# Optimization experiments

Measured on AMD Instinct MI355X. Metric: run time of the kernel, lower is better.

## Reference

```python
import jax, jax.numpy as jnp
import numpy as np

B, S, D = 4, 2048, 1024
H = 16
HD = D // H  # 64


def setup_inputs() -> dict:
    key = jax.random.key(0)
    kx, kq, kp = jax.random.split(key, 3)
    x = jax.random.normal(kx, (B, S, D), dtype=jnp.float32)
    # torch Linear weights are [out, in]; match init scale ~ U(-1/sqrt(in), 1/sqrt(in))
    lim = 1.0 / np.sqrt(D)
    w_qkv = jax.random.uniform(kq, (3 * D, D), dtype=jnp.float32, minval=-lim, maxval=lim)
    w_proj = jax.random.uniform(kp, (D, D), dtype=jnp.float32, minval=-lim, maxval=lim)
    return {"x": x, "w_qkv": w_qkv, "w_proj": w_proj}


def reference(x, w_qkv, w_proj):
    b, s, d = x.shape
    qkv = jnp.einsum('bsd,ed->bse', x, w_qkv)  # [B,S,3D]
    q, k, v = jnp.split(qkv, 3, axis=-1)
    # [B,H,S,HD]
    q = q.reshape(b, s, H, HD).transpose(0, 2, 1, 3)
    k = k.reshape(b, s, H, HD).transpose(0, 2, 1, 3)
    v = v.reshape(b, s, H, HD).transpose(0, 2, 1, 3)
    scale = 1.0 / np.sqrt(HD)
    attn = jnp.einsum('bhqd,bhkd->bhqk', q, k) * scale  # [B,H,S,S]
    causal = jnp.tril(jnp.ones((s, s), dtype=bool))
    attn = jnp.where(causal[None, None], attn, -jnp.inf)
    attn = jax.nn.softmax(attn, axis=-1)
    out = jnp.einsum('bhqk,bhkd->bhqd', attn, v)
    out = out.transpose(0, 2, 1, 3).reshape(b, s, d)
    return jnp.einsum('bsd,ed->bse', out, w_proj)
```

## Files before the change

kernel.cpp:

```cpp
#include <hip/hip_runtime.h>

typedef unsigned short u16;
typedef unsigned int u32;

#define B_ 4
#define S_ 2048
#define D_ 1024
#define H_ 16
#define HD_ 64
#define M_ (B_ * S_)
#define QK_ (2 * D_)
#define NP_ 32

typedef __bf16 bf16x8 __attribute__((ext_vector_type(8)));
typedef float f32x4 __attribute__((ext_vector_type(4)));

#define MASKVAL (-1.0e30f)
#define RESCALE_THR 8.0f

static __device__ __forceinline__ u16 f2bf_hw(float f) {
    union { __bf16 b; u16 u; } v;
    v.b = (__bf16)f;
    return v.u;
}

static __device__ __forceinline__ void gload16(const u16* g, u16* l) {
    __builtin_amdgcn_global_load_lds(
        (const __attribute__((address_space(1))) void*)g,
        (__attribute__((address_space(3))) void*)l, 16, 0, 0);
}

__global__ __launch_bounds__(256) void cvt_bf16(const float* __restrict__ src,
                                                u16* __restrict__ dst) {
    size_t i = ((size_t)blockIdx.x * 256 + threadIdx.x) * 8;
    float4 a = *(const float4*)(src + i);
    float4 b = *(const float4*)(src + i + 4);
    union { u16 h[8]; int4 v; } pk;
    pk.h[0] = f2bf_hw(a.x); pk.h[1] = f2bf_hw(a.y);
    pk.h[2] = f2bf_hw(a.z); pk.h[3] = f2bf_hw(a.w);
    pk.h[4] = f2bf_hw(b.x); pk.h[5] = f2bf_hw(b.y);
    pk.h[6] = f2bf_hw(b.z); pk.h[7] = f2bf_hw(b.w);
    *(int4*)(dst + i) = pk.v;
}

template <int EPI, int BM, int TPB>
__global__ __launch_bounds__(TPB, (TPB == 512) ? 4 : 2)
void gemm8p(const u16* __restrict__ A, const u16* __restrict__ Bw,
            void* __restrict__ Cout, void* __restrict__ C2, int Ndim) {
    __shared__ u16 As[3][BM * 32];
    __shared__ u16 Bs[3][128 * 32];
    constexpr int LA = (BM * 4) / TPB;
    constexpr int LB = 512 / TPB;
    constexpr int L = LA + LB;
    const int t = threadIdx.x;
    const int wave = t >> 6, lane = t & 63;
    const int ml = lane & 15, quad = lane >> 4;
    const int wr = wave >> 1, wc = wave & 1;
    const int bx = blockIdx.x, by = blockIdx.y;
    const int rowA0 = by * BM, rowB0 = bx * 128;

    f32x4 acc[4][4];
    const f32x4 zero = {0.f, 0.f, 0.f, 0.f};
#pragma unroll
    for (int i = 0; i < 4; ++i)
#pragma unroll
        for (int j = 0; j < 4; ++j) acc[i][j] = zero;

    auto STAGE = [&](int slot, int pnl) {
        const int colbase = pnl * 32;
#pragma unroll
        for (int l = 0; l < LA; ++l) {
            const int base = l * TPB + wave * 64;
            const int idx = base + lane;
            const int row = idx >> 2;
            const int sch = ((idx & 3) ^ ((idx >> 3) & 3)) * 8;
            gload16(&A[(size_t)(rowA0 + row) * 1024 + colbase + sch],
                    &As[slot][base * 8]);
        }
#pragma unroll
        for (int l = 0; l < LB; ++l) {
            const int base = l * TPB + wave * 64;
            const int idx = base + lane;
            const int row = idx >> 2;
            const int sch = ((idx & 3) ^ ((idx >> 3) & 3)) * 8;
            gload16(&Bw[(size_t)(rowB0 + row) * 1024 + colbase + sch],
                    &Bs[slot][base * 8]);
        }
    };

    STAGE(0, 0);
    STAGE(1, 1);
    if constexpr (L == 3) { asm volatile("s_waitcnt vmcnt(3)" ::: "memory"); }
    else                  { asm volatile("s_waitcnt vmcnt(4)" ::: "memory"); }
    __builtin_amdgcn_s_barrier();

    for (int p = 0; p < NP_; ++p) {
        const int slot = p % 3;
        bf16x8 a[4], b[4];
#pragma unroll
        for (int i = 0; i < 4; ++i) {
            const int row = wr * 64 + i * 16 + ml;
            a[i] = *(const bf16x8*)(&As[slot][row * 32 + ((quad ^ ((row >> 1) & 3)) << 3)]);
        }
#pragma unroll
        for (int j = 0; j < 4; ++j) {
            const int row = wc * 64 + j * 16 + ml;
            b[j] = *(const bf16x8*)(&Bs[slot][row * 32 + ((quad ^ ((row >> 1) & 3)) << 3)]);
        }
        if (p + 2 < NP_) STAGE((p + 2) % 3, p + 2);
        __builtin_amdgcn_s_barrier();
        asm volatile("s_waitcnt lgkmcnt(0)" ::: "memory");
        __builtin_amdgcn_sched_barrier(0);
        __builtin_amdgcn_s_setprio(1);
#pragma unroll
        for (int i = 0; i < 4; ++i)
#pragma unroll
            for (int j = 0; j < 4; ++j)
                acc[i][j] = __builtin_amdgcn_mfma_f32_16x16x32_bf16(a[i], b[j], acc[i][j], 0, 0, 0);
        __builtin_amdgcn_s_setprio(0);
        if (p + 2 < NP_) {
            if constexpr (L == 3) { asm volatile("s_waitcnt vmcnt(3)" ::: "memory"); }
            else                  { asm volatile("s_waitcnt vmcnt(4)" ::: "memory"); }
        } else {
            asm volatile("s_waitcnt vmcnt(0)" ::: "memory");
        }
        __builtin_amdgcn_s_barrier();
    }

    if constexpr (EPI == 2) {
        float* C = (float*)Cout;
#pragma unroll
        for (int i = 0; i < 4; ++i)
#pragma unroll
            for (int j = 0; j < 4; ++j)
#pragma unroll
                for (int r = 0; r < 4; ++r) {
                    int row = rowA0 + wr * 64 + i * 16 + quad * 4 + r;
                    int col = rowB0 + wc * 64 + j * 16 + ml;
                    C[(size_t)row * Ndim + col] = acc[i][j][r];
                }
    } else {
        if (bx < 16) {
            u16* C = (u16*)Cout;
#pragma unroll
            for (int i = 0; i < 4; ++i)
#pragma unroll
                for (int j = 0; j < 4; ++j)
#pragma unroll
                    for (int r = 0; r < 4; ++r) {
                        int row = rowA0 + wr * 64 + i * 16 + quad * 4 + r;
                        int col = rowB0 + wc * 64 + j * 16 + ml;
                        C[(size_t)row * Ndim + col] = f2bf_hw(acc[i][j][r]);
                    }
        } else {
            u16* Vt = (u16*)C2;
#pragma unroll
            for (int i = 0; i < 4; ++i)
#pragma unroll
                for (int j = 0; j < 4; ++j) {
                    int row0 = rowA0 + wr * 64 + i * 16 + quad * 4;
                    int col = rowB0 + wc * 64 + j * 16 + ml - 2048;
                    int b = row0 >> 11;
                    int s0 = row0 & (S_ - 1);
                    union { u16 h[4]; ushort4 v; } pk;
#pragma unroll
                    for (int r = 0; r < 4; ++r) pk.h[r] = f2bf_hw(acc[i][j][r]);
                    *(ushort4*)(&Vt[((size_t)(b * D_ + col)) * S_ + s0]) = pk.v;
                }
        }
    }
}

__global__ __launch_bounds__(256, 3) void attn3(const u16* __restrict__ qk,
                                                const u16* __restrict__ Vt,
                                                u16* __restrict__ AO) {
    __shared__ u16 Klds[2][64 * 64];
    __shared__ u16 Vlds[2][64 * 64];
    __shared__ u16 Pw[4][32 * 72];
    const int t = threadIdx.x;
    const int wave = t >> 6, lane = t & 63;
    const int ml = lane & 15, quad = lane >> 4;
    const int mhx = (ml & 8) >> 1;

    const int jj = blockIdx.x >> 6;
    const int bh = blockIdx.x & 63;
    const int t4 = jj >> 2, r4 = jj & 3;
    const int j = (t4 < 2) ? (15 - 4 * t4 - r4) : (12 - 4 * t4 + r4);
    const int b = bh >> 4, h = bh & 15;
    const size_t rowbase = (size_t)b * S_;

    const int srow8 = lane >> 3;
    const int schunk = ((lane & 7) ^ srow8) * 8;

    const int qj0 = j * 128 + wave * 32;
    const int ktw = 2 * j + (wave >> 1);
    const int ktmax = 2 * j + 1;

    u16* pwb = &Pw[wave][0];

    bf16x8 qf[2][2];
#pragma unroll
    for (int mi = 0; mi < 2; ++mi)
#pragma unroll
        for (int kc = 0; kc < 2; ++kc) {
            bf16x8 q = *(const bf16x8*)(&qk[(rowbase + qj0 + mi * 16 + ml) * QK_ +
                                            h * HD_ + kc * 32 + quad * 8]);
#pragma unroll
            for (int e = 0; e < 8; ++e) {
                float f = (float)q[e] * 0.125f;
                q[e] = (__bf16)f;
            }
            qf[mi][kc] = q;
        }

    f32x4 o[2][4];
    float m[2], ls[2];
    const f32x4 zero = {0.f, 0.f, 0.f, 0.f};
#pragma unroll
    for (int mi = 0; mi < 2; ++mi) {
#pragma unroll
        for (int nd = 0; nd < 4; ++nd) o[mi][nd] = zero;
        m[mi] = MASKVAL; ls[mi] = 0.f;
    }

    bf16x8 vf[4][2];

    auto STAGE = [&](int buf, int kt) {
        const int kb = kt * 64;
#pragma unroll
        for (int p = 0; p < 2; ++p) {
            const int rbase = wave * 16 + p * 8;
            gload16(&qk[(rowbase + kb + rbase + srow8) * QK_ + D_ + h * HD_ + schunk],
                    &Klds[buf][rbase * 64]);
            gload16(&Vt[(size_t)(bh * HD_ + rbase + srow8) * S_ + kb + schunk],
                    &Vlds[buf][rbase * 64]);
        }
    };

    auto PV = [&]() {
        bf16x8 pf[2][2];
#pragma unroll
        for (int mi = 0; mi < 2; ++mi)
#pragma unroll
            for (int kc = 0; kc < 2; ++kc)
                pf[mi][kc] = *(const bf16x8*)(&pwb[(mi * 16 + ml) * 72 +
                                                   (((kc * 4 + quad) ^ mhx) << 3)]);
        __builtin_amdgcn_s_setprio(1);
#pragma unroll
        for (int mi = 0; mi < 2; ++mi)
#pragma unroll
            for (int nd = 0; nd < 4; ++nd)
#pragma unroll
                for (int kc = 0; kc < 2; ++kc)
                    o[mi][nd] = __builtin_amdgcn_mfma_f32_16x16x32_bf16(pf[mi][kc], vf[nd][kc],
                                                                        o[mi][nd], 0, 0, 0);
        __builtin_amdgcn_s_setprio(0);
    };

    STAGE(0, 0);

    for (int kt = 0; kt <= ktmax; ++kt) {
        const int cur = kt & 1;
        if (kt < ktmax) STAGE(cur ^ 1, kt + 1);

        if (kt >= 1 && kt - 1 <= ktw) PV();

        if (kt < ktmax) {
            asm volatile("s_waitcnt vmcnt(4)" ::: "memory");
        } else {
            asm volatile("s_waitcnt vmcnt(0)" ::: "memory");
        }
        __builtin_amdgcn_s_barrier();

        if (kt <= ktw) {
            const int kb = kt * 64;
            f32x4 sc[2][4];
            __builtin_amdgcn_s_setprio(1);
#pragma unroll
            for (int ni = 0; ni < 4; ++ni) {
                const int row = ni * 16 + ml;
                bf16x8 kfa = *(const bf16x8*)(&Klds[cur][row * 64 + ((quad ^ (ml & 7)) << 3)]);
                bf16x8 kfb = *(const bf16x8*)(&Klds[cur][row * 64 + (((4 + quad) ^ (ml & 7)) << 3)]);
#pragma unroll
                for (int mi = 0; mi < 2; ++mi) {
                    f32x4 s = __builtin_amdgcn_mfma_f32_16x16x32_bf16(kfa, qf[mi][0], zero, 0, 0, 0);
                    sc[mi][ni] = __builtin_amdgcn_mfma_f32_16x16x32_bf16(kfb, qf[mi][1], s, 0, 0, 0);
                }
            }
            __builtin_amdgcn_s_setprio(0);

            if (kb + 63 > qj0) {
#pragma unroll
                for (int mi = 0; mi < 2; ++mi) {
                    const int q = qj0 + mi * 16 + ml;
#pragma unroll
                    for (int ni = 0; ni < 4; ++ni)
#pragma unroll
                        for (int r = 0; r < 4; ++r) {
                            int k = kb + ni * 16 + quad * 4 + r;
                            if (k > q) sc[mi][ni][r] = MASKVAL;
                        }
                }
            }

#pragma unroll
            for (int mi = 0; mi < 2; ++mi) {
                float tm = sc[mi][0][0];
#pragma unroll
                for (int ni = 0; ni < 4; ++ni)
#pragma unroll
                    for (int r = 0; r < 4; ++r) tm = fmaxf(tm, sc[mi][ni][r]);
                tm = fmaxf(tm, __shfl_xor(tm, 16, 64));
                tm = fmaxf(tm, __shfl_xor(tm, 32, 64));
                if (__any(tm > m[mi] + RESCALE_THR)) {
                    float mn = fmaxf(m[mi], tm);
                    float al = __expf(m[mi] - mn);
                    m[mi] = mn;
                    ls[mi] *= al;
                    float alr[4];
#pragma unroll
                    for (int r = 0; r < 4; ++r)
                        alr[r] = __shfl(al, (lane & 48) + ((lane & 48) >> 2) + r, 64);
#pragma unroll
                    for (int nd = 0; nd < 4; ++nd)
#pragma unroll
                        for (int r = 0; r < 4; ++r) o[mi][nd][r] *= alr[r];
                }
                float sum = 0.f;
#pragma unroll
                for (int ni = 0; ni < 4; ++ni)
#pragma unroll
                    for (int r = 0; r < 4; ++r) {
                        float e = __expf(sc[mi][ni][r] - m[mi]);
                        sc[mi][ni][r] = e;
                        sum += e;
                    }
                ls[mi] += sum;
#pragma unroll
                for (int ni = 0; ni < 4; ++ni) {
                    union { u16 h[4]; ushort4 v; } pk;
#pragma unroll
                    for (int r = 0; r < 4; ++r) pk.h[r] = f2bf_hw(sc[mi][ni][r]);
                    const int off = (mi * 16 + ml) * 72 +
                                    ((((2 * ni + (quad >> 1)) ^ mhx)) << 3) + ((quad & 1) << 2);
                    *(ushort4*)(&pwb[off]) = pk.v;
                }
            }
#pragma unroll
            for (int ni = 0; ni < 4; ++ni) {
                const int row = ni * 16 + ml;
#pragma unroll
                for (int kc = 0; kc < 2; ++kc)
                    vf[ni][kc] = *(const bf16x8*)(&Vlds[cur][row * 64 +
                                                            (((kc * 4 + quad) ^ (ml & 7)) << 3)]);
            }
        }
        asm volatile("s_waitcnt lgkmcnt(0)" ::: "memory");
        __builtin_amdgcn_s_barrier();
    }

    if (ktw == ktmax) PV();

#pragma unroll
    for (int mi = 0; mi < 2; ++mi) {
        float s = ls[mi];
        s += __shfl_xor(s, 16, 64);
        s += __shfl_xor(s, 32, 64);
        float rl = 1.0f / s;
        float rlr[4];
#pragma unroll
        for (int r = 0; r < 4; ++r)
            rlr[r] = __shfl(rl, (lane & 48) + ((lane & 48) >> 2) + r, 64);
#pragma unroll
        for (int nd = 0; nd < 4; ++nd)
#pragma unroll
            for (int r = 0; r < 4; ++r) {
                int srow = qj0 + mi * 16 + quad * 4 + r;
                AO[(rowbase + srow) * D_ + h * HD_ + nd * 16 + ml] =
                    f2bf_hw(o[mi][nd][r] * rlr[r]);
            }
    }
}

__global__ __launch_bounds__(256) void copy16(const int4* __restrict__ src,
                                              int4* __restrict__ dst) {
    size_t i = (size_t)blockIdx.x * 256 + threadIdx.x;
    dst[i] = src[i];
}

extern "C" void kernel_launch(void* const* d_in, const int* in_sizes, int n_in,
                              void* d_out, int out_size, void* d_ws, size_t ws_size,
                              hipStream_t stream) {
    const float* x = (const float*)d_in[0];
    const float* wqkv = (const float*)d_in[1];
    const float* wproj = (const float*)d_in[2];
    float* out = (float*)d_out;

    u16* qkw = (u16*)d_ws;
    u16* Vtw = qkw + (size_t)M_ * QK_;

    u16* xb = (u16*)d_out;
    u16* wprojb = xb + (size_t)M_ * D_;
    u16* wqkvb = wprojb + (size_t)D_ * D_;

    const size_t need = ((size_t)M_ * QK_ + 8388608  + (size_t)M_ * D_  +
                         (size_t)D_ * D_ ) * sizeof(u16);
    const bool bigws = ws_size >= need;
    u16* AOb    = bigws ? (Vtw + (size_t)8388608) : xb;
    u16* wprojd = bigws ? (AOb + (size_t)M_ * D_) : wprojb;
    u16* AOp    = bigws ? AOb : qkw;
    u16* wprojp = bigws ? wprojd : qkw + (size_t)M_ * D_;

    cvt_bf16<<<dim3(M_ * D_ / 2048), 256, 0, stream>>>(x, xb);
    cvt_bf16<<<dim3(D_ * D_ / 2048), 256, 0, stream>>>(wproj, wprojd);
    cvt_bf16<<<dim3(3 * D_ * D_ / 2048), 256, 0, stream>>>(wqkv, wqkvb);

    gemm8p<3, 256, 512><<<dim3(3 * D_ / 128, M_ / 256), 512, 0, stream>>>(
        xb, wqkvb, qkw, Vtw, QK_);
    attn3<<<dim3(1024), 256, 0, stream>>>(qkw, Vtw, AOb);
    if (!bigws) {
        copy16<<<dim3((unsigned)(((size_t)M_ * D_ + (size_t)D_ * D_) * 2 / (256 * 16))),
                 256, 0, stream>>>((const int4*)AOb, (int4*)qkw);
    }
    gemm8p<2, 128, 256><<<dim3(D_ / 128, M_ / 128), 256, 0, stream>>>(
        AOp, wprojp, out, nullptr, D_);
}
```

Baseline: 244.9 us.

## Write attention output in place into the Q buffer and fuse conversions

The attention kernel now writes its output into the dead Q columns of the qk workspace. The projection GEMM then reads that buffer through a stride argument, and the converted wproj is placed in the V buffer once attention is done. This drops the workspace-size branching and the copy kernel. The x and wqkv conversions are merged into one launch, one LDS barrier per GEMM k-step is removed, and softmax exponentials move to exp2 with a folded log2(e) FMA. The in-place reuse depends on each attention block reading only its own Q rows before overwriting them, and the removed barrier assumes the trailing barrier is enough to protect the staging slot.

Result: no change. 244.3 us (-0.3%).

```diff
diff --git a/kernel.cpp b/kernel.cpp
--- a/kernel.cpp
+++ b/kernel.cpp
@@ -11,6 +11,7 @@
 #define M_ (B_ * S_)
 #define QK_ (2 * D_)
 #define NP_ 32
+#define LOG2E 1.442695041f
 
 typedef __bf16 bf16x8 __attribute__((ext_vector_type(8)));
 typedef float f32x4 __attribute__((ext_vector_type(4)));
@@ -30,9 +31,10 @@
         (__attribute__((address_space(3))) void*)l, 16, 0, 0);
 }
 
-__global__ __launch_bounds__(256) void cvt_bf16(const float* __restrict__ src,
-                                                u16* __restrict__ dst) {
-    size_t i = ((size_t)blockIdx.x * 256 + threadIdx.x) * 8;
+static __device__ __forceinline__ void cvt_body(const float* __restrict__ src,
+                                                u16* __restrict__ dst, size_t blk,
+                                                int tid) {
+    size_t i = (blk * 256 + tid) * 8;
     float4 a = *(const float4*)(src + i);
     float4 b = *(const float4*)(src + i + 4);
     union { u16 h[8]; int4 v; } pk;
@@ -43,10 +45,25 @@
     *(int4*)(dst + i) = pk.v;
 }
 
+__global__ __launch_bounds__(256) void cvt_xw(const float* __restrict__ x,
+                                              const float* __restrict__ wqkv,
+                                              u16* __restrict__ xb,
+                                              u16* __restrict__ wqkvb) {
+    int bid = blockIdx.x;
+    if (bid < 4096) cvt_body(x, xb, bid, threadIdx.x);
+    else            cvt_body(wqkv, wqkvb, bid - 4096, threadIdx.x);
+}
+
+__global__ __launch_bounds__(256) void cvt_one(const float* __restrict__ src,
+                                               u16* __restrict__ dst) {
+    cvt_body(src, dst, blockIdx.x, threadIdx.x);
+}
+
 template <int EPI, int BM, int TPB>
 __global__ __launch_bounds__(TPB, (TPB == 512) ? 4 : 2)
 void gemm8p(const u16* __restrict__ A, const u16* __restrict__ Bw,
-            void* __restrict__ Cout, void* __restrict__ C2, int Ndim) {
+            void* __restrict__ Cout, void* __restrict__ C2,
+            int Ndim, int strideA, int strideB) {
     __shared__ u16 As[3][BM * 32];
     __shared__ u16 Bs[3][128 * 32];
     constexpr int LA = (BM * 4) / TPB;
@@ -74,7 +91,7 @@
             const int idx = base + lane;
             const int row = idx >> 2;
             const int sch = ((idx & 3) ^ ((idx >> 3) & 3)) * 8;
-            gload16(&A[(size_t)(rowA0 + row) * 1024 + colbase + sch],
+            gload16(&A[(size_t)(rowA0 + row) * strideA + colbase + sch],
                     &As[slot][base * 8]);
         }
 #pragma unroll
@@ -83,7 +100,7 @@
             const int idx = base + lane;
             const int row = idx >> 2;
             const int sch = ((idx & 3) ^ ((idx >> 3) & 3)) * 8;
-            gload16(&Bw[(size_t)(rowB0 + row) * 1024 + colbase + sch],
+            gload16(&Bw[(size_t)(rowB0 + row) * strideB + colbase + sch],
                     &Bs[slot][base * 8]);
         }
     };
@@ -108,7 +125,6 @@
             b[j] = *(const bf16x8*)(&Bs[slot][row * 32 + ((quad ^ ((row >> 1) & 3)) << 3)]);
         }
         if (p + 2 < NP_) STAGE((p + 2) % 3, p + 2);
-        __builtin_amdgcn_s_barrier();
         asm volatile("s_waitcnt lgkmcnt(0)" ::: "memory");
         __builtin_amdgcn_sched_barrier(0);
         __builtin_amdgcn_s_setprio(1);
@@ -171,9 +187,8 @@
     }
 }
 
-__global__ __launch_bounds__(256, 3) void attn3(const u16* __restrict__ qk,
-                                                const u16* __restrict__ Vt,
-                                                u16* __restrict__ AO) {
+__global__ __launch_bounds__(256, 3) void attn3(u16* __restrict__ qk,
+                                                const u16* __restrict__ Vt) {
     __shared__ u16 Klds[2][64 * 64];
     __shared__ u16 Vlds[2][64 * 64];
     __shared__ u16 Pw[4][32 * 72];
@@ -314,7 +329,7 @@
                 tm = fmaxf(tm, __shfl_xor(tm, 32, 64));
                 if (__any(tm > m[mi] + RESCALE_THR)) {
                     float mn = fmaxf(m[mi], tm);
-                    float al = __expf(m[mi] - mn);
+                    float al = __builtin_amdgcn_exp2f((m[mi] - mn) * LOG2E);
                     m[mi] = mn;
                     ls[mi] *= al;
                     float alr[4];
@@ -326,12 +341,13 @@
 #pragma unroll
                         for (int r = 0; r < 4; ++r) o[mi][nd][r] *= alr[r];
                 }
+                const float mm = m[mi] * LOG2E;
                 float sum = 0.f;
 #pragma unroll
                 for (int ni = 0; ni < 4; ++ni)
 #pragma unroll
                     for (int r = 0; r < 4; ++r) {
-                        float e = __expf(sc[mi][ni][r] - m[mi]);
+                        float e = __builtin_amdgcn_exp2f(__builtin_fmaf(sc[mi][ni][r], LOG2E, -mm));
                         sc[mi][ni][r] = e;
                         sum += e;
                     }
@@ -376,16 +392,10 @@
 #pragma unroll
             for (int r = 0; r < 4; ++r) {
                 int srow = qj0 + mi * 16 + quad * 4 + r;
-                AO[(rowbase + srow) * D_ + h * HD_ + nd * 16 + ml] =
+                qk[(rowbase + srow) * QK_ + h * HD_ + nd * 16 + ml] =
                     f2bf_hw(o[mi][nd][r] * rlr[r]);
             }
     }
-}
-
-__global__ __launch_bounds__(256) void copy16(const int4* __restrict__ src,
-                                              int4* __restrict__ dst) {
-    size_t i = (size_t)blockIdx.x * 256 + threadIdx.x;
-    dst[i] = src[i];
 }
 
 extern "C" void kernel_launch(void* const* d_in, const int* in_sizes, int n_in,
@@ -400,28 +410,17 @@
     u16* Vtw = qkw + (size_t)M_ * QK_;
 
     u16* xb = (u16*)d_out;
-    u16* wprojb = xb + (size_t)M_ * D_;
-    u16* wqkvb = wprojb + (size_t)D_ * D_;
-
-    const size_t need = ((size_t)M_ * QK_ + 8388608  + (size_t)M_ * D_  +
-                         (size_t)D_ * D_ ) * sizeof(u16);
-    const bool bigws = ws_size >= need;
-    u16* AOb    = bigws ? (Vtw + (size_t)8388608) : xb;
-    u16* wprojd = bigws ? (AOb + (size_t)M_ * D_) : wprojb;
-    u16* AOp    = bigws ? AOb : qkw;
-    u16* wprojp = bigws ? wprojd : qkw + (size_t)M_ * D_;
-
-    cvt_bf16<<<dim3(M_ * D_ / 2048), 256, 0, stream>>>(x, xb);
-    cvt_bf16<<<dim3(D_ * D_ / 2048), 256, 0, stream>>>(wproj, wprojd);
-    cvt_bf16<<<dim3(3 * D_ * D_ / 2048), 256, 0, stream>>>(wqkv, wqkvb);
+    u16* wqkvb = xb + (size_t)M_ * D_;
+
+    cvt_xw<<<dim3(4096 + 1536), 256, 0, stream>>>(x, wqkv, xb, wqkvb);
 
     gemm8p<3, 256, 512><<<dim3(3 * D_ / 128, M_ / 256), 512, 0, stream>>>(
-        xb, wqkvb, qkw, Vtw, QK_);
-    attn3<<<dim3(1024), 256, 0, stream>>>(qkw, Vtw, AOb);
-    if (!bigws) {
-        copy16<<<dim3((unsigned)(((size_t)M_ * D_ + (size_t)D_ * D_) * 2 / (256 * 16))),
-                 256, 0, stream>>>((const int4*)AOb, (int4*)qkw);
-    }
+        xb, wqkvb, qkw, Vtw, QK_, D_, D_);
+
+    attn3<<<dim3(1024), 256, 0, stream>>>(qkw, Vtw);
+
+    cvt_one<<<dim3(512), 256, 0, stream>>>(wproj, Vtw);
+
     gemm8p<2, 128, 256><<<dim3(D_ / 128, M_ / 128), 256, 0, stream>>>(
-        AOp, wprojp, out, nullptr, D_);
-}
+        qkw, Vtw, out, nullptr, D_, QK_, D_);
+}
```
